# Optimization experiments

Measured on AMD Instinct MI355X. Metric: run time of the kernel, lower is better.

## Reference

```python
import jax, jax.numpy as jnp
import numpy as np

N, E = 100000, 1600000
IN, H, OUT, EA = 128, 128, 128, 128
NUM_LAYERS = 4
EPS = 1e-5


def setup_inputs() -> dict:
    key = jax.random.key(0)
    ks = jax.random.split(key, 12)
    s = 0.05  # small init scale for numerical sanity
    inp = {
        "x": jax.random.normal(ks[0], (N, IN), jnp.float32),
        "edge_index": jax.random.randint(ks[1], (2, E), 0, N, dtype=jnp.int32),
        "edge_attr": jax.random.normal(ks[2], (E, EA), jnp.float32),
        # MLP linears: in->H, H->H, H->H, H->OUT
        "W0": jax.random.normal(ks[3], (H, IN), jnp.float32) * s,
        "b0": jnp.zeros((H,), jnp.float32),
        "W1": jax.random.normal(ks[4], (H, H), jnp.float32) * s,
        "b1": jnp.zeros((H,), jnp.float32),
        "W2": jax.random.normal(ks[5], (H, H), jnp.float32) * s,
        "b2": jnp.zeros((H,), jnp.float32),
        "W3": jax.random.normal(ks[6], (OUT, H), jnp.float32) * s,
        "b3": jnp.zeros((OUT,), jnp.float32),
        # EdgeConv linear: concat(x_j[H], edge_attr[EA]) -> H
        "Wc": jax.random.normal(ks[7], (H, H + EA), jnp.float32) * s,
        "bc": jnp.zeros((H,), jnp.float32),
        # BatchNorm (eval mode: running stats)
        "bn_gamma": jnp.ones((H,), jnp.float32),
        "bn_beta": jnp.zeros((H,), jnp.float32),
        "bn_mean": jnp.zeros((H,), jnp.float32),
        "bn_var": jnp.ones((H,), jnp.float32),
    }
    return inp


def _edge_conv(h, src, dst, ea, deg_inv, Wc, bc):
    # message: lin(concat(x_j, edge_attr)) per edge; aggregate: mean over dst
    msg = jnp.concatenate([h[src], ea], axis=1) @ Wc.T + bc  # [E+N, H]
    agg = jax.ops.segment_sum(msg, dst, num_segments=N)      # [N, H]
    return agg * deg_inv[:, None]


def reference(x, edge_index, edge_attr, W0, b0, W1, b1, W2, b2, W3, b3,
              Wc, bc, bn_gamma, bn_beta, bn_mean, bn_var):
    loop = jnp.arange(N, dtype=edge_index.dtype)
    src = jnp.concatenate([edge_index[0], loop])  # self-loops appended
    dst = jnp.concatenate([edge_index[1], loop])
    ea = jnp.concatenate([edge_attr, jnp.zeros((N, EA), edge_attr.dtype)], axis=0)
    deg = jax.ops.segment_sum(jnp.ones((src.shape[0],), x.dtype), dst, num_segments=N)
    deg_inv = 1.0 / deg  # >= 1 thanks to self-loops

    layers = [(W0, b0), (W1, b1), (W2, b2), (W3, b3)]
    h = x
    for i, (W, b) in enumerate(layers):
        h = h @ W.T                                   # [N, H]
        h = _edge_conv(h, src, dst, ea, deg_inv, Wc, bc)  # eval-mode propagation
        h = h + b
        if i != NUM_LAYERS - 1:
            # BatchNorm1d eval: normalize by running stats
            h = (h - bn_mean) * jax.lax.rsqrt(bn_var + EPS) * bn_gamma + bn_beta
            h = jnp.tanh(h)
            # dropout p=0.0 / eval mode: no-op
    return h
```

## Files before the change

### kernel.cpp

```cpp
#include <hip/hip_runtime.h>
#include <hip/hip_bf16.h>
#include <math.h>

#define NN 100000
#define EE 1600000
#define HD 128
#define MAXDEG 128
#define EPS_BN 1e-5f

typedef __attribute__((ext_vector_type(8))) short short8;
typedef __attribute__((ext_vector_type(4))) float f32x4;

__device__ inline float bf_hi(unsigned u) { return __uint_as_float(u & 0xffff0000u); }
__device__ inline float bf_lo(unsigned u) { return __uint_as_float(u << 16); }
__device__ inline unsigned pack_bf2(float x0, float x1) {
    __hip_bfloat16 a = __float2bfloat16(x0);
    __hip_bfloat16 b = __float2bfloat16(x1);
    unsigned short ua = *reinterpret_cast<unsigned short*>(&a);
    unsigned short ub = *reinterpret_cast<unsigned short*>(&b);
    return (unsigned)ua | ((unsigned)ub << 16);
}

__global__ __launch_bounds__(256) void mega_k(const float* __restrict__ x, unsigned* __restrict__ xb,
                                              const int* __restrict__ src, const int* __restrict__ dst,
                                              int* __restrict__ cursor, int2* __restrict__ list,
                                              const float* __restrict__ W0, const float* __restrict__ W1,
                                              const float* __restrict__ W2, const float* __restrict__ W3,
                                              const float* __restrict__ Wc,
                                              __hip_bfloat16* __restrict__ Mb,
                                              __hip_bfloat16* __restrict__ Wceb) {
    int t = blockIdx.x * 256 + threadIdx.x;
    {
        size_t base = (size_t)t * 8;
        float4 a = *(const float4*)&x[base];
        float4 b = *(const float4*)&x[base + 4];
        uint4 w;
        w.x = pack_bf2(a.x, a.y); w.y = pack_bf2(a.z, a.w);
        w.z = pack_bf2(b.x, b.y); w.w = pack_bf2(b.z, b.w);
        *(uint4*)&xb[(size_t)t * 4] = w;
    }
    {
        int v = dst[t];
        int p = atomicAdd(&cursor[v], 1);
        if (p < MAXDEG) list[(size_t)v * MAXDEG + p] = make_int2(t, src[t]);
    }
    if (blockIdx.x < 320) {
        int part = blockIdx.x >> 6;
        int idx = ((blockIdx.x & 63) << 8) + threadIdx.x;
        int o = idx >> 7, k = idx & 127;
        if (part < 4) {
            const float* W = (part == 0) ? W0 : (part == 1) ? W1 : (part == 2) ? W2 : W3;
            float s = 0.f;
            for (int j = 0; j < 128; ++j) s += Wc[o * 256 + j] * W[j * 128 + k];
            Mb[part * 16384 + idx] = __float2bfloat16(s);
        } else {
            Wceb[idx] = __float2bfloat16(Wc[o * 256 + 128 + k]);
        }
    }
}

__global__ __launch_bounds__(256) void agg_ea_k(const float* __restrict__ ea,
                                                const int* __restrict__ deg, const int2* __restrict__ list,
                                                unsigned* __restrict__ A) {
    int v = blockIdx.x * 4 + (threadIdx.x >> 6);
    int lane = threadIdx.x & 63;
    int grp = lane >> 5, lr = lane & 31;
    if (v >= NN) return;
    size_t o = (size_t)v * MAXDEG;
    int d = deg[v];
    float a0 = 0.f, a1 = 0.f, a2 = 0.f, a3 = 0.f;
    float c0 = 0.f, c1 = 0.f, c2 = 0.f, c3 = 0.f;
    int j = grp;
    for (; j + 6 < d; j += 8) {
        int e0 = list[o + j].x;
        int e1 = list[o + j + 2].x;
        int e2 = list[o + j + 4].x;
        int e3 = list[o + j + 6].x;
        float4 r0 = *(const float4*)&ea[(size_t)e0 * HD + lr * 4];
        float4 r1 = *(const float4*)&ea[(size_t)e1 * HD + lr * 4];
        float4 r2 = *(const float4*)&ea[(size_t)e2 * HD + lr * 4];
        float4 r3 = *(const float4*)&ea[(size_t)e3 * HD + lr * 4];
        a0 += r0.x + r1.x; a1 += r0.y + r1.y; a2 += r0.z + r1.z; a3 += r0.w + r1.w;
        c0 += r2.x + r3.x; c1 += r2.y + r3.y; c2 += r2.z + r3.z; c3 += r2.w + r3.w;
    }
    for (; j + 2 < d; j += 4) {
        int e0 = list[o + j].x;
        int e1 = list[o + j + 2].x;
        float4 r0 = *(const float4*)&ea[(size_t)e0 * HD + lr * 4];
        float4 r1 = *(const float4*)&ea[(size_t)e1 * HD + lr * 4];
        a0 += r0.x + r1.x; a1 += r0.y + r1.y; a2 += r0.z + r1.z; a3 += r0.w + r1.w;
    }
    for (; j < d; j += 2) {
        int e = list[o + j].x;
        float4 r = *(const float4*)&ea[(size_t)e * HD + lr * 4];
        a0 += r.x; a1 += r.y; a2 += r.z; a3 += r.w;
    }
    a0 += c0; a1 += c1; a2 += c2; a3 += c3;
    a0 += __shfl_xor(a0, 32); a1 += __shfl_xor(a1, 32);
    a2 += __shfl_xor(a2, 32); a3 += __shfl_xor(a3, 32);
    if (grp == 0) {
        uint2 w;
        w.x = pack_bf2(a0, a1); w.y = pack_bf2(a2, a3);
        *(uint2*)&A[(size_t)v * 64 + lr * 2] = w;
    }
}

__global__ __launch_bounds__(256) void gather_sum_k(const unsigned* __restrict__ tab,
                                                    const int* __restrict__ deg, const int2* __restrict__ list,
                                                    unsigned* __restrict__ S) {
    int v = blockIdx.x * 4 + (threadIdx.x >> 6);
    int lane = threadIdx.x & 63;
    int grp = lane >> 4, lr = lane & 15;
    if (v >= NN) return;
    size_t o = (size_t)v * MAXDEG;
    int d = deg[v];
    float acc[8], acc2[8];
    {
        uint4 r = *(const uint4*)&tab[(size_t)v * 64 + lr * 4];
        bool m = (grp == 0);
        acc[0] = m ? bf_lo(r.x) : 0.f; acc[1] = m ? bf_hi(r.x) : 0.f;
        acc[2] = m ? bf_lo(r.y) : 0.f; acc[3] = m ? bf_hi(r.y) : 0.f;
        acc[4] = m ? bf_lo(r.z) : 0.f; acc[5] = m ? bf_hi(r.z) : 0.f;
        acc[6] = m ? bf_lo(r.w) : 0.f; acc[7] = m ? bf_hi(r.w) : 0.f;
    }
#pragma unroll
    for (int i = 0; i < 8; ++i) acc2[i] = 0.f;
    int j = grp;
    for (; j + 12 < d; j += 16) {
        int s0 = list[o + j].y;
        int s1 = list[o + j + 4].y;
        int s2 = list[o + j + 8].y;
        int s3 = list[o + j + 12].y;
        uint4 r0 = *(const uint4*)&tab[(size_t)s0 * 64 + lr * 4];
        uint4 r1 = *(const uint4*)&tab[(size_t)s1 * 64 + lr * 4];
        uint4 r2 = *(const uint4*)&tab[(size_t)s2 * 64 + lr * 4];
        uint4 r3 = *(const uint4*)&tab[(size_t)s3 * 64 + lr * 4];
        acc[0] += bf_lo(r0.x) + bf_lo(r1.x); acc[1] += bf_hi(r0.x) + bf_hi(r1.x);
        acc[2] += bf_lo(r0.y) + bf_lo(r1.y); acc[3] += bf_hi(r0.y) + bf_hi(r1.y);
        acc[4] += bf_lo(r0.z) + bf_lo(r1.z); acc[5] += bf_hi(r0.z) + bf_hi(r1.z);
        acc[6] += bf_lo(r0.w) + bf_lo(r1.w); acc[7] += bf_hi(r0.w) + bf_hi(r1.w);
        acc2[0] += bf_lo(r2.x) + bf_lo(r3.x); acc2[1] += bf_hi(r2.x) + bf_hi(r3.x);
        acc2[2] += bf_lo(r2.y) + bf_lo(r3.y); acc2[3] += bf_hi(r2.y) + bf_hi(r3.y);
        acc2[4] += bf_lo(r2.z) + bf_lo(r3.z); acc2[5] += bf_hi(r2.z) + bf_hi(r3.z);
        acc2[6] += bf_lo(r2.w) + bf_lo(r3.w); acc2[7] += bf_hi(r2.w) + bf_hi(r3.w);
    }
    for (; j + 4 < d; j += 8) {
        int s0 = list[o + j].y;
        int s1 = list[o + j + 4].y;
        uint4 r0 = *(const uint4*)&tab[(size_t)s0 * 64 + lr * 4];
        uint4 r1 = *(const uint4*)&tab[(size_t)s1 * 64 + lr * 4];
        acc[0] += bf_lo(r0.x) + bf_lo(r1.x); acc[1] += bf_hi(r0.x) + bf_hi(r1.x);
        acc[2] += bf_lo(r0.y) + bf_lo(r1.y); acc[3] += bf_hi(r0.y) + bf_hi(r1.y);
        acc[4] += bf_lo(r0.z) + bf_lo(r1.z); acc[5] += bf_hi(r0.z) + bf_hi(r1.z);
        acc[6] += bf_lo(r0.w) + bf_lo(r1.w); acc[7] += bf_hi(r0.w) + bf_hi(r1.w);
    }
    for (; j < d; j += 4) {
        int s = list[o + j].y;
        uint4 r = *(const uint4*)&tab[(size_t)s * 64 + lr * 4];
        acc[0] += bf_lo(r.x); acc[1] += bf_hi(r.x);
        acc[2] += bf_lo(r.y); acc[3] += bf_hi(r.y);
        acc[4] += bf_lo(r.z); acc[5] += bf_hi(r.z);
        acc[6] += bf_lo(r.w); acc[7] += bf_hi(r.w);
    }
#pragma unroll
    for (int i = 0; i < 8; ++i) {
        acc[i] += acc2[i];
        acc[i] += __shfl_xor(acc[i], 16);
        acc[i] += __shfl_xor(acc[i], 32);
    }
    if (grp == 0) {
        uint4 w;
        w.x = pack_bf2(acc[0], acc[1]); w.y = pack_bf2(acc[2], acc[3]);
        w.z = pack_bf2(acc[4], acc[5]); w.w = pack_bf2(acc[6], acc[7]);
        *(uint4*)&S[(size_t)v * 64 + lr * 4] = w;
    }
}

template <int MODE>
__global__ __launch_bounds__(256) void gemm_epi_k(const __hip_bfloat16* __restrict__ Sb,
                                                  const __hip_bfloat16* __restrict__ Bw,
                                                  const __hip_bfloat16* __restrict__ Ub,
                                                  const int* __restrict__ deg,
                                                  const float* __restrict__ bias,
                                                  const float* __restrict__ bng, const float* __restrict__ bnb,
                                                  const float* __restrict__ bnm, const float* __restrict__ bnv,
                                                  void* __restrict__ out) {
    int wave = threadIdx.x >> 6, lane = threadIdx.x & 63;
    int r0 = blockIdx.x * 64 + wave * 16;
    int lr = lane & 15, lg = lane >> 4;

    f32x4 acc[8];
#pragma unroll
    for (int i = 0; i < 8; ++i) acc[i] = (f32x4){0.f, 0.f, 0.f, 0.f};

    int arow = r0 + lr;
    if (arow >= NN) arow = NN - 1;

#pragma unroll
    for (int kb = 0; kb < 4; ++kb) {
        int kofs = kb * 32 + lg * 8;
        short8 a = *(const short8*)(Sb + (size_t)arow * HD + kofs);
#pragma unroll
        for (int fr = 0; fr < 8; ++fr) {
            short8 b = *(const short8*)(Bw + (size_t)(fr * 16 + lr) * HD + kofs);
            acc[fr] = __builtin_amdgcn_mfma_f32_16x16x32_bf16(a, b, acc[fr], 0, 0, 0);
        }
    }

    float di[4];
#pragma unroll
    for (int j = 0; j < 4; ++j) {
        int grow = r0 + lg * 4 + j;
        int d = deg[(grow < NN) ? grow : (NN - 1)];
        di[j] = 1.0f / (float)(d + 1);
    }
#pragma unroll
    for (int fr = 0; fr < 8; ++fr) {
        int col = fr * 16 + lr;
        float bs = bias[col];
        float me = 0.f, sc = 0.f, be = 0.f;
        if (MODE == 1) {
            me = bnm[col];
            sc = bng[col] * rsqrtf(bnv[col] + EPS_BN);
            be = bnb[col];
        }
#pragma unroll
        for (int j = 0; j < 4; ++j) {
            int grow = r0 + lg * 4 + j;
            if (grow >= NN) continue;
            float val = acc[fr][j] * di[j] + bs;
            if (MODE != 0) val += __bfloat162float(Ub[(size_t)grow * HD + col]);
            if (MODE == 1) {
                val = tanhf((val - me) * sc + be);
            }
            if (MODE == 2) {
                ((float*)out)[(size_t)grow * HD + col] = val;
            } else {
                ((__hip_bfloat16*)out)[(size_t)grow * HD + col] = __float2bfloat16(val);
            }
        }
    }
}

extern "C" void kernel_launch(void* const* d_in, const int* in_sizes, int n_in,
                              void* d_out, int out_size, void* d_ws, size_t ws_size,
                              hipStream_t stream) {
    const float* x   = (const float*)d_in[0];
    const int*   ei  = (const int*)d_in[1];
    const float* ea  = (const float*)d_in[2];
    const float* W0  = (const float*)d_in[3];
    const float* b0  = (const float*)d_in[4];
    const float* W1  = (const float*)d_in[5];
    const float* b1  = (const float*)d_in[6];
    const float* W2  = (const float*)d_in[7];
    const float* b2  = (const float*)d_in[8];
    const float* W3  = (const float*)d_in[9];
    const float* b3  = (const float*)d_in[10];
    const float* Wc  = (const float*)d_in[11];
    const float* bc  = (const float*)d_in[12];
    const float* bng = (const float*)d_in[13];
    const float* bnb = (const float*)d_in[14];
    const float* bnm = (const float*)d_in[15];
    const float* bnv = (const float*)d_in[16];

    const int* ei0 = ei;
    const int* ei1 = ei + EE;

    char* ws = (char*)d_ws;
    int*   cursor  = (int*)(ws + 0);
    __hip_bfloat16* Mb   = (__hip_bfloat16*)(ws + 400128);
    __hip_bfloat16* Wceb = (__hip_bfloat16*)(ws + 531200);
    int2*  list    = (int2*)(ws + 564224);
    unsigned* A_b  = (unsigned*)(ws + 102964224);
    unsigned* U_b  = (unsigned*)(ws + 128564224);
    unsigned* S_b  = (unsigned*)(ws + 154164224);
    unsigned* h_b  = (unsigned*)(ws + 179764224);
    unsigned* x_b  = (unsigned*)(ws + 205364224);
    (void)ws_size; (void)in_sizes; (void)n_in; (void)out_size;

    hipMemsetAsync(cursor, 0, 400000, stream);

    mega_k<<<EE / 256, 256, 0, stream>>>(x, x_b, ei0, ei1, cursor, list,
                                         W0, W1, W2, W3, Wc, Mb, Wceb);

    agg_ea_k<<<NN / 4, 256, 0, stream>>>(ea, cursor, list, A_b);

    int gblocks = (NN + 63) / 64;
    gemm_epi_k<0><<<gblocks, 256, 0, stream>>>((const __hip_bfloat16*)A_b, Wceb, nullptr,
                                               cursor, bc, nullptr, nullptr, nullptr, nullptr,
                                               (void*)U_b);

    const float* biases[4] = {b0, b1, b2, b3};
    for (int layer = 0; layer < 4; ++layer) {
        const unsigned* tab = (layer == 0) ? x_b : h_b;
        gather_sum_k<<<NN / 4, 256, 0, stream>>>(tab, cursor, list, S_b);
        if (layer < 3) {
            gemm_epi_k<1><<<gblocks, 256, 0, stream>>>((const __hip_bfloat16*)S_b, Mb + layer * 16384,
                                                       (const __hip_bfloat16*)U_b, cursor, biases[layer],
                                                       bng, bnb, bnm, bnv, (void*)h_b);
        } else {
            gemm_epi_k<2><<<gblocks, 256, 0, stream>>>((const __hip_bfloat16*)S_b, Mb + layer * 16384,
                                                       (const __hip_bfloat16*)U_b, cursor, biases[layer],
                                                       nullptr, nullptr, nullptr, nullptr, d_out);
        }
    }
}
```

Measured before the change: 753.9 us.

## Fold edge-attr GEMM into per-layer K=256 GEMM and co-launch first gather

The separate U = A·Wce GEMM and its bf16 buffer are removed. Each layer's GEMM now runs with K=256 over the concatenation [S | A] against a concatenated weight [Wc_x·W_l | Wc_e], and bc is added in the epilogue. The edge-attribute aggregation and the first-layer gather are merged into one launch by interleaving blocks. This drops one GEMM launch and the per-layer read of U, but adds an extra A read and twice the MFMA work in every layer GEMM.

```diff
diff --git a/kernel.cpp b/kernel.cpp
--- a/kernel.cpp
+++ b/kernel.cpp
@@ -27,8 +27,7 @@
                                               const float* __restrict__ W0, const float* __restrict__ W1,
                                               const float* __restrict__ W2, const float* __restrict__ W3,
                                               const float* __restrict__ Wc,
-                                              __hip_bfloat16* __restrict__ Mb,
-                                              __hip_bfloat16* __restrict__ Wceb) {
+                                              __hip_bfloat16* __restrict__ Mcat) {
     int t = blockIdx.x * 256 + threadIdx.x;
     {
         size_t base = (size_t)t * 8;
@@ -44,28 +43,22 @@
         int p = atomicAdd(&cursor[v], 1);
         if (p < MAXDEG) list[(size_t)v * MAXDEG + p] = make_int2(t, src[t]);
     }
-    if (blockIdx.x < 320) {
+    if (blockIdx.x < 256) {
         int part = blockIdx.x >> 6;
         int idx = ((blockIdx.x & 63) << 8) + threadIdx.x;
         int o = idx >> 7, k = idx & 127;
-        if (part < 4) {
-            const float* W = (part == 0) ? W0 : (part == 1) ? W1 : (part == 2) ? W2 : W3;
-            float s = 0.f;
-            for (int j = 0; j < 128; ++j) s += Wc[o * 256 + j] * W[j * 128 + k];
-            Mb[part * 16384 + idx] = __float2bfloat16(s);
-        } else {
-            Wceb[idx] = __float2bfloat16(Wc[o * 256 + 128 + k]);
-        }
-    }
-}
-
-__global__ __launch_bounds__(256) void agg_ea_k(const float* __restrict__ ea,
-                                                const int* __restrict__ deg, const int2* __restrict__ list,
-                                                unsigned* __restrict__ A) {
-    int v = blockIdx.x * 4 + (threadIdx.x >> 6);
-    int lane = threadIdx.x & 63;
+        const float* W = (part == 0) ? W0 : (part == 1) ? W1 : (part == 2) ? W2 : W3;
+        float s = 0.f;
+        for (int j = 0; j < 128; ++j) s += Wc[o * 256 + j] * W[j * 128 + k];
+        Mcat[part * 32768 + o * 256 + k]       = __float2bfloat16(s);
+        Mcat[part * 32768 + o * 256 + 128 + k] = __float2bfloat16(Wc[o * 256 + 128 + k]);
+    }
+}
+
+__device__ __forceinline__ void agg_ea_node(const float* __restrict__ ea, const int* __restrict__ deg,
+                                            const int2* __restrict__ list, unsigned* __restrict__ A,
+                                            int v, int lane) {
     int grp = lane >> 5, lr = lane & 31;
-    if (v >= NN) return;
     size_t o = (size_t)v * MAXDEG;
     int d = deg[v];
     float a0 = 0.f, a1 = 0.f, a2 = 0.f, a3 = 0.f;
@@ -105,13 +98,10 @@
     }
 }
 
-__global__ __launch_bounds__(256) void gather_sum_k(const unsigned* __restrict__ tab,
-                                                    const int* __restrict__ deg, const int2* __restrict__ list,
-                                                    unsigned* __restrict__ S) {
-    int v = blockIdx.x * 4 + (threadIdx.x >> 6);
-    int lane = threadIdx.x & 63;
+__device__ __forceinline__ void gather_node(const unsigned* __restrict__ tab, const int* __restrict__ deg,
+                                            const int2* __restrict__ list, unsigned* __restrict__ S,
+                                            int v, int lane) {
     int grp = lane >> 4, lr = lane & 15;
-    if (v >= NN) return;
     size_t o = (size_t)v * MAXDEG;
     int d = deg[v];
     float acc[8], acc2[8];
@@ -176,15 +166,35 @@
     }
 }
 
+__global__ __launch_bounds__(256) void combo_k(const float* __restrict__ ea, const unsigned* __restrict__ xb,
+                                               const int* __restrict__ deg, const int2* __restrict__ list,
+                                               unsigned* __restrict__ A, unsigned* __restrict__ S) {
+    int v = (blockIdx.x >> 1) * 4 + (threadIdx.x >> 6);
+    int lane = threadIdx.x & 63;
+    if (v >= NN) return;
+    if (blockIdx.x & 1) gather_node(xb, deg, list, S, v, lane);
+    else                agg_ea_node(ea, deg, list, A, v, lane);
+}
+
+__global__ __launch_bounds__(256) void gather_sum_k(const unsigned* __restrict__ tab,
+                                                    const int* __restrict__ deg, const int2* __restrict__ list,
+                                                    unsigned* __restrict__ S) {
+    int v = blockIdx.x * 4 + (threadIdx.x >> 6);
+    int lane = threadIdx.x & 63;
+    if (v >= NN) return;
+    gather_node(tab, deg, list, S, v, lane);
+}
+
 template <int MODE>
-__global__ __launch_bounds__(256) void gemm_epi_k(const __hip_bfloat16* __restrict__ Sb,
-                                                  const __hip_bfloat16* __restrict__ Bw,
-                                                  const __hip_bfloat16* __restrict__ Ub,
-                                                  const int* __restrict__ deg,
-                                                  const float* __restrict__ bias,
-                                                  const float* __restrict__ bng, const float* __restrict__ bnb,
-                                                  const float* __restrict__ bnm, const float* __restrict__ bnv,
-                                                  void* __restrict__ out) {
+__global__ __launch_bounds__(256) void gemm256_k(const __hip_bfloat16* __restrict__ Sb,
+                                                 const __hip_bfloat16* __restrict__ Ab,
+                                                 const __hip_bfloat16* __restrict__ Bcat,
+                                                 const int* __restrict__ deg,
+                                                 const float* __restrict__ bc,
+                                                 const float* __restrict__ bias,
+                                                 const float* __restrict__ bng, const float* __restrict__ bnb,
+                                                 const float* __restrict__ bnm, const float* __restrict__ bnv,
+                                                 void* __restrict__ out) {
     int wave = threadIdx.x >> 6, lane = threadIdx.x & 63;
     int r0 = blockIdx.x * 64 + wave * 16;
     int lr = lane & 15, lg = lane >> 4;
@@ -197,12 +207,14 @@
     if (arow >= NN) arow = NN - 1;
 
 #pragma unroll
-    for (int kb = 0; kb < 4; ++kb) {
+    for (int kb = 0; kb < 8; ++kb) {
+        int aofs = (kb & 3) * 32 + lg * 8;
+        const __hip_bfloat16* At = (kb < 4) ? Sb : Ab;
+        short8 a = *(const short8*)(At + (size_t)arow * HD + aofs);
         int kofs = kb * 32 + lg * 8;
-        short8 a = *(const short8*)(Sb + (size_t)arow * HD + kofs);
 #pragma unroll
         for (int fr = 0; fr < 8; ++fr) {
-            short8 b = *(const short8*)(Bw + (size_t)(fr * 16 + lr) * HD + kofs);
+            short8 b = *(const short8*)(Bcat + (size_t)(fr * 16 + lr) * 256 + kofs);
             acc[fr] = __builtin_amdgcn_mfma_f32_16x16x32_bf16(a, b, acc[fr], 0, 0, 0);
         }
     }
@@ -217,7 +229,7 @@
 #pragma unroll
     for (int fr = 0; fr < 8; ++fr) {
         int col = fr * 16 + lr;
-        float bs = bias[col];
+        float bs = bc[col] + bias[col];
         float me = 0.f, sc = 0.f, be = 0.f;
         if (MODE == 1) {
             me = bnm[col];
@@ -229,14 +241,11 @@
             int grow = r0 + lg * 4 + j;
             if (grow >= NN) continue;
             float val = acc[fr][j] * di[j] + bs;
-            if (MODE != 0) val += __bfloat162float(Ub[(size_t)grow * HD + col]);
             if (MODE == 1) {
                 val = tanhf((val - me) * sc + be);
-            }
-            if (MODE == 2) {
+                ((__hip_bfloat16*)out)[(size_t)grow * HD + col] = __float2bfloat16(val);
+            } else {
                 ((float*)out)[(size_t)grow * HD + col] = val;
-            } else {
-                ((__hip_bfloat16*)out)[(size_t)grow * HD + col] = __float2bfloat16(val);
             }
         }
     }
@@ -268,40 +277,35 @@
 
     char* ws = (char*)d_ws;
     int*   cursor  = (int*)(ws + 0);
-    __hip_bfloat16* Mb   = (__hip_bfloat16*)(ws + 400128);
-    __hip_bfloat16* Wceb = (__hip_bfloat16*)(ws + 531200);
-    int2*  list    = (int2*)(ws + 564224);
-    unsigned* A_b  = (unsigned*)(ws + 102964224);
-    unsigned* U_b  = (unsigned*)(ws + 128564224);
-    unsigned* S_b  = (unsigned*)(ws + 154164224);
-    unsigned* h_b  = (unsigned*)(ws + 179764224);
-    unsigned* x_b  = (unsigned*)(ws + 205364224);
+    __hip_bfloat16* Mcat = (__hip_bfloat16*)(ws + 400128);
+    int2*  list    = (int2*)(ws + 662272);
+    unsigned* A_b  = (unsigned*)(ws + 103062272);
+    unsigned* S_b  = (unsigned*)(ws + 128662272);
+    unsigned* h_b  = (unsigned*)(ws + 154262272);
+    unsigned* x_b  = (unsigned*)(ws + 179862272);
     (void)ws_size; (void)in_sizes; (void)n_in; (void)out_size;
 
     hipMemsetAsync(cursor, 0, 400000, stream);
 
     mega_k<<<EE / 256, 256, 0, stream>>>(x, x_b, ei0, ei1, cursor, list,
-                                         W0, W1, W2, W3, Wc, Mb, Wceb);
-
-    agg_ea_k<<<NN / 4, 256, 0, stream>>>(ea, cursor, list, A_b);
+                                         W0, W1, W2, W3, Wc, Mcat);
+
+    combo_k<<<(NN / 4) * 2, 256, 0, stream>>>(ea, x_b, cursor, list, A_b, S_b);
 
     int gblocks = (NN + 63) / 64;
-    gemm_epi_k<0><<<gblocks, 256, 0, stream>>>((const __hip_bfloat16*)A_b, Wceb, nullptr,
-                                               cursor, bc, nullptr, nullptr, nullptr, nullptr,
-                                               (void*)U_b);
-
     const float* biases[4] = {b0, b1, b2, b3};
     for (int layer = 0; layer < 4; ++layer) {
-        const unsigned* tab = (layer == 0) ? x_b : h_b;
-        gather_sum_k<<<NN / 4, 256, 0, stream>>>(tab, cursor, list, S_b);
+        if (layer > 0) {
+            gather_sum_k<<<NN / 4, 256, 0, stream>>>(h_b, cursor, list, S_b);
+        }
         if (layer < 3) {
-            gemm_epi_k<1><<<gblocks, 256, 0, stream>>>((const __hip_bfloat16*)S_b, Mb + layer * 16384,
-                                                       (const __hip_bfloat16*)U_b, cursor, biases[layer],
-                                                       bng, bnb, bnm, bnv, (void*)h_b);
+            gemm256_k<1><<<gblocks, 256, 0, stream>>>((const __hip_bfloat16*)S_b, (const __hip_bfloat16*)A_b,
+                                                      Mcat + layer * 32768, cursor, bc, biases[layer],
+                                                      bng, bnb, bnm, bnv, (void*)h_b);
         } else {
-            gemm_epi_k<2><<<gblocks, 256, 0, stream>>>((const __hip_bfloat16*)S_b, Mb + layer * 16384,
-                                                       (const __hip_bfloat16*)U_b, cursor, biases[layer],
-                                                       nullptr, nullptr, nullptr, nullptr, d_out);
-        }
-    }
-}
+            gemm256_k<2><<<gblocks, 256, 0, stream>>>((const __hip_bfloat16*)S_b, (const __hip_bfloat16*)A_b,
+                                                      Mcat + layer * 32768, cursor, bc, biases[layer],
+                                                      nullptr, nullptr, nullptr, nullptr, d_out);
+        }
+    }
+}
```

Result: slower. 769.1 us (+2.0%).
